# Performance work log

Hardware: AMD Instinct MI355X
Metric: run time of the kernel (lower is better)

The kernel has to match this reference:

```python
import jax, jax.numpy as jnp
import numpy as np

N = 50000      # nodes
E_RAND = 800000
IN = 256       # in_dim
HID = 64       # num_hidden
H = 4          # heads for GATv2 layers 0,1
C = 32         # num_classes (final layer, 1 head)
SLOPE = 0.2


def setup_inputs() -> dict:
    key = jax.random.key(0)
    ks = jax.random.split(key, 12)
    x = jax.random.normal(ks[0], (N, IN), dtype=jnp.float32)
    src = jax.random.randint(ks[1], (E_RAND,), 0, N, dtype=jnp.int32)
    dst = jax.random.randint(ks[2], (E_RAND,), 0, N, dtype=jnp.int32)
    loops = jnp.arange(N, dtype=jnp.int32)  # self-loops: every node has an in-edge
    src = jnp.concatenate([src, loops])
    dst = jnp.concatenate([dst, loops])
    s = 0.05
    W0 = jax.random.normal(ks[3], (IN, H * HID), dtype=jnp.float32) * s
    a0 = jax.random.normal(ks[4], (H, HID), dtype=jnp.float32) * s
    W1 = jax.random.normal(ks[5], (H * HID, H * HID), dtype=jnp.float32) * s
    a1 = jax.random.normal(ks[6], (H, HID), dtype=jnp.float32) * s
    W2 = jax.random.normal(ks[7], (H * HID, 1 * C), dtype=jnp.float32) * s
    a2 = jax.random.normal(ks[8], (1, C), dtype=jnp.float32) * s
    Wres2 = jax.random.normal(ks[9], (H * HID, C), dtype=jnp.float32) * s
    return {"x": x, "src": src, "dst": dst, "W0": W0, "a0": a0,
            "W1": W1, "a1": a1, "W2": W2, "a2": a2, "Wres2": Wres2}


def _gatv2_layer(h, W, a, src, dst, heads, out, res, activation):
    n = h.shape[0]
    # share_weights=True: same projection for src and dst (DGL GATv2Conv)
    f = (h @ W).reshape(n, heads, out)            # [N,H,D]
    fe = f[src] + f[dst]                          # gather: [E,H,D]
    e = jnp.einsum('ehd,hd->eh', jax.nn.leaky_relu(fe, SLOPE), a)  # [E,H]
    # edge softmax over incoming edges per destination node
    m = jax.ops.segment_max(e, dst, num_segments=n)
    ex = jnp.exp(e - m[dst])
    z = jax.ops.segment_sum(ex, dst, num_segments=n)
    alpha = ex / z[dst]                           # [E,H]
    msg = alpha[:, :, None] * f[src]              # [E,H,D]
    rst = jax.ops.segment_sum(msg, dst, num_segments=n)  # [N,H,D]
    if res is not None:
        rst = rst + res
    if activation:
        rst = jax.nn.elu(rst)
    return rst


def reference(x, src, dst, W0, a0, W1, a1, W2, a2, Wres2):
    # layer 0: no residual, elu, flatten heads
    h = _gatv2_layer(x, W0, a0, src, dst, H, HID, None, True).reshape(N, H * HID)
    # layer 1: residual (in == heads*out -> identity reshape), elu, flatten
    res1 = h.reshape(N, H, HID)
    h = _gatv2_layer(h, W1, a1, src, dst, H, HID, res1, True).reshape(N, H * HID)
    # final layer: residual via res_fc (256 != 1*32), no activation, mean over heads
    res2 = (h @ Wres2).reshape(N, 1, C)
    logits = _gatv2_layer(h, W2, a2, src, dst, 1, C, res2, False).mean(axis=1)
    return logits
```

## Files before the change

### kernel.cpp

```cpp
#include <hip/hip_runtime.h>
#include <hip/hip_bf16.h>

typedef __hip_bfloat16 bf16;
#define SLOPE 0.2f

typedef _Float16 h2v __attribute__((ext_vector_type(2)));
typedef _Float16 h8v __attribute__((ext_vector_type(8)));
typedef __attribute__((ext_vector_type(8))) short bf16x8;
typedef __attribute__((ext_vector_type(16))) float f32x16;

__device__ __forceinline__ float b2f(bf16 v) { return __bfloat162float(v); }
__device__ __forceinline__ short f2b_raw(float x) {
    bf16 b = __float2bfloat16(x);
    return *reinterpret_cast<short*>(&b);
}
__device__ __forceinline__ short f2h_raw(float x) {
    _Float16 h = (_Float16)x;
    return *reinterpret_cast<short*>(&h);
}
__device__ __forceinline__ h2v u2h(unsigned u) {
    union { unsigned x; h2v h; } c; c.x = u; return c.h;
}

template <int CTRL>
__device__ __forceinline__ float dpp_radd(float x) {
    int y = __builtin_amdgcn_update_dpp(0, __float_as_int(x), CTRL, 0xF, 0xF, false);
    return x + __int_as_float(y);
}
#define DPP_QUAD_XOR1 0xB1
#define DPP_QUAD_XOR2 0x4E
#define DPP_ROR1 0x121
#define DPP_ROR2 0x122
#define DPP_ROR4 0x124
#define DPP_ROR8 0x128

union Q16 { uint4 q[2]; unsigned u[8]; };

__global__ void k_prep(const void* __restrict__ x,
                       const void* __restrict__ W0, const void* __restrict__ W1,
                       const void* __restrict__ W2, const void* __restrict__ Wr2,
                       const void* __restrict__ a0, const void* __restrict__ a1,
                       const void* __restrict__ a2, short* __restrict__ W0p,
                       short* __restrict__ W1p, short* __restrict__ W2fp,
                       short* __restrict__ a0c, short* __restrict__ a1c,
                       short* __restrict__ a2c, int* __restrict__ flag,
                       int* __restrict__ cnt, int* __restrict__ ticket, int N) {
    __shared__ int sflag;
    if (threadIdx.x < 64) {
        const unsigned short* u = (const unsigned short*)x;
        int tid = threadIdx.x;
        int nice = 0;
        for (int k = tid; k < 256; k += 64) {
            unsigned int bits = ((unsigned int)u[2 * k]) << 16;
            float v = __uint_as_float(bits);
            float av = fabsf(v);
            if (v == 0.0f || (av > 1e-6f && av < 100.0f)) ++nice;
        }
        for (int off = 32; off > 0; off >>= 1) nice += __shfl_down(nice, off, 64);
        if (tid == 0) sflag = (nice >= 192) ? 0 : 1;
    }
    __syncthreads();
    int isf = sflag;
    int idx = blockIdx.x * blockDim.x + threadIdx.x;
    if (blockIdx.x == 0 && threadIdx.x == 0) { *flag = isf; *ticket = 0; }
    if (idx < N) cnt[idx] = 0;
    if (idx < 131072) {
        int t = idx & 65535;
        int j = t & 7, L = (t >> 3) & 63, kt = (t >> 9) & 15, nt = t >> 13;
        int n = nt * 32 + (L & 31);
        int k = kt * 16 + (L >> 5) * 8 + j;
        const void* src = (idx < 65536) ? W0 : W1;
        float v = isf ? ((const float*)src)[k * 256 + n] : b2f(((const bf16*)src)[k * 256 + n]);
        short* dstp = (idx < 65536) ? W0p : W1p;
        dstp[t] = f2h_raw(v);
    } else if (idx < 147456) {
        int t = idx - 131072;
        int j = t & 7, L = (t >> 3) & 63, kt = (t >> 9) & 15, nt = t >> 13;
        int n = nt * 32 + (L & 31);
        int k = kt * 16 + (L >> 5) * 8 + j;
        const void* src = (n < 32) ? W2 : Wr2;
        int nn = n & 31;
        float v = isf ? ((const float*)src)[k * 32 + nn] : b2f(((const bf16*)src)[k * 32 + nn]);
        W2fp[t] = f2h_raw(v);
    } else if (idx < 147456 + 256) {
        int t = idx - 147456;
        float v = isf ? ((const float*)a0)[t] : b2f(((const bf16*)a0)[t]);
        a0c[t] = f2h_raw(v);
    } else if (idx < 147456 + 512) {
        int t = idx - 147456 - 256;
        float v = isf ? ((const float*)a1)[t] : b2f(((const bf16*)a1)[t]);
        a1c[t] = f2h_raw(v);
    } else if (idx < 147456 + 544) {
        int t = idx - 147456 - 512;
        float v = isf ? ((const float*)a2)[t] : b2f(((const bf16*)a2)[t]);
        a2c[t] = f2h_raw(v);
    }
}

__global__ void k_hist(const int* __restrict__ dst, int* __restrict__ cnt, int E) {
    int e = blockIdx.x * blockDim.x + threadIdx.x;
    if (e < E) atomicAdd(&cnt[dst[e]], 1);
}

__global__ void k_bsum_scan(const int* __restrict__ cnt, int* __restrict__ bsum,
                            int* __restrict__ ticket, int n, int B) {
    __shared__ int sh[256];
    __shared__ int lastFlag;
    int base = blockIdx.x * 1024 + threadIdx.x * 4;
    int s = 0;
#pragma unroll
    for (int k = 0; k < 4; ++k) { int i = base + k; if (i < n) s += cnt[i]; }
    sh[threadIdx.x] = s;
    __syncthreads();
    for (int off = 128; off > 0; off >>= 1) {
        if (threadIdx.x < off) sh[threadIdx.x] += sh[threadIdx.x + off];
        __syncthreads();
    }
    if (threadIdx.x == 0) {
        atomicExch(&bsum[blockIdx.x], sh[0]);
        __threadfence();
        int t = atomicAdd(ticket, 1);
        lastFlag = (t == B - 1) ? 1 : 0;
    }
    __syncthreads();
    if (lastFlag && threadIdx.x < 64) {
        int tid = threadIdx.x;
        int v = (tid < B) ? atomicAdd(&bsum[tid], 0) : 0;
        int xv = v;
#pragma unroll
        for (int off = 1; off < 64; off <<= 1) {
            int y = __shfl_up(xv, off, 64);
            if (tid >= off) xv += y;
        }
        if (tid < B) bsum[tid] = xv - v;
    }
}

__global__ void k_scanwrite(const int* __restrict__ cnt, const int* __restrict__ bsum,
                            int* __restrict__ rowptr, int* __restrict__ cursor, int n, int E) {
    __shared__ int sh[256];
    int base = blockIdx.x * 1024 + threadIdx.x * 4;
    int loc[4];
    int s = 0;
#pragma unroll
    for (int k = 0; k < 4; ++k) {
        int i = base + k;
        loc[k] = (i < n) ? cnt[i] : 0;
        s += loc[k];
    }
    sh[threadIdx.x] = s;
    __syncthreads();
    for (int off = 1; off < 256; off <<= 1) {
        int u = (threadIdx.x >= off) ? sh[threadIdx.x - off] : 0;
        __syncthreads();
        sh[threadIdx.x] += u;
        __syncthreads();
    }
    int run = bsum[blockIdx.x] + sh[threadIdx.x] - s;
#pragma unroll
    for (int k = 0; k < 4; ++k) {
        int i = base + k;
        if (i < n) { rowptr[i] = run; cursor[i] = run; run += loc[k]; }
    }
    if (blockIdx.x == 0 && threadIdx.x == 0) rowptr[n] = E;
}

__global__ void k_scatter(const int* __restrict__ src, const int* __restrict__ dst,
                          int* __restrict__ cursor, int* __restrict__ csr_src, int E) {
    int e = blockIdx.x * blockDim.x + threadIdx.x;
    if (e < E) {
        int p = atomicAdd(&cursor[dst[e]], 1);
        csr_src[p] = src[e];
    }
}

template <int ADAPT>
__global__ void k_gemm_mfma(const void* __restrict__ A, const short* __restrict__ Wp,
                            short* __restrict__ C, int Nrows, const int* __restrict__ flag) {
    __shared__ short sA[64 * 264];
    int tid = threadIdx.x;
    int warp = tid >> 6;
    int lane = tid & 63;
    long blockRow = (long)blockIdx.x * 64;
    int isf32 = ADAPT ? *flag : 0;

    if (ADAPT && isf32) {
        const float* Af = (const float*)A;
#pragma unroll
        for (int it = 0; it < 16; ++it) {
            int linear = it * 256 + tid;
            int row = linear >> 6;
            int col4 = linear & 63;
            long gr = blockRow + row;
            if (gr > Nrows - 1) gr = Nrows - 1;
            float4 v = ((const float4*)(Af + gr * 256))[col4];
            short* d = &sA[row * 264 + col4 * 4];
            d[0] = f2h_raw(v.x); d[1] = f2h_raw(v.y);
            d[2] = f2h_raw(v.z); d[3] = f2h_raw(v.w);
        }
    } else if (ADAPT) {
        const short* Ab = (const short*)A;
#pragma unroll
        for (int it = 0; it < 8; ++it) {
            int linear = it * 256 + tid;
            int row = linear >> 5;
            int c8 = linear & 31;
            long gr = blockRow + row;
            if (gr > Nrows - 1) gr = Nrows - 1;
            bf16x8 v = *(const bf16x8*)(Ab + gr * 256 + c8 * 8);
            short* d = &sA[row * 264 + c8 * 8];
#pragma unroll
            for (int k = 0; k < 8; ++k) {
                unsigned bits = ((unsigned)(unsigned short)v[k]) << 16;
                d[k] = f2h_raw(__uint_as_float(bits));
            }
        }
    } else {
        const short* Ab = (const short*)A;
#pragma unroll
        for (int it = 0; it < 8; ++it) {
            int linear = it * 256 + tid;
            int row = linear >> 5;
            int c8 = linear & 31;
            long gr = blockRow + row;
            if (gr > Nrows - 1) gr = Nrows - 1;
            bf16x8 v = *(const bf16x8*)(Ab + gr * 256 + c8 * 8);
            *(bf16x8*)&sA[row * 264 + c8 * 8] = v;
        }
    }
    __syncthreads();

    int wr = warp >> 1;
    int wc = warp & 1;
    long rowBase = blockRow + wr * 32;
    int colBase = wc * 128;
    int m = lane & 31;
    int g = lane >> 5;
    int smemRow = wr * 32 + m;
    f32x16 acc[4] = {};
    for (int kt = 0; kt < 16; ++kt) {
        h8v af = *(const h8v*)&sA[smemRow * 264 + kt * 16 + g * 8];
#pragma unroll
        for (int ct = 0; ct < 4; ++ct) {
            int nt = wc * 4 + ct;
            h8v bfr = *(const h8v*)(Wp + (((nt << 4) + kt) << 9) + lane * 8);
            acc[ct] = __builtin_amdgcn_mfma_f32_32x32x16_f16(af, bfr, acc[ct], 0, 0, 0);
        }
    }
#pragma unroll
    for (int ct = 0; ct < 4; ++ct) {
#pragma unroll
        for (int i = 0; i < 16; ++i) {
            long row = rowBase + (i & 3) + 8 * (i >> 2) + 4 * g;
            if (row < Nrows)
                C[row * 256 + colBase + ct * 32 + m] = f2h_raw(acc[ct][i]);
        }
    }
}

__global__ void k_gemm_mfma64(const short* __restrict__ A, const short* __restrict__ Wp,
                              short* __restrict__ C, int Nrows) {
    int warp = threadIdx.x >> 6;
    int lane = threadIdx.x & 63;
    long rowBase = (long)blockIdx.x * 128 + warp * 32;
    int m = lane & 31;
    int g = lane >> 5;
    long r = rowBase + m;
    if (r >= Nrows) r = Nrows - 1;
    const short* Arow = A + r * 256 + g * 8;
    f32x16 acc[2] = {};
    for (int kt = 0; kt < 16; ++kt) {
        h8v af = *(const h8v*)(Arow + kt * 16);
#pragma unroll
        for (int ct = 0; ct < 2; ++ct) {
            h8v bfr = *(const h8v*)(Wp + (((ct << 4) + kt) << 9) + lane * 8);
            acc[ct] = __builtin_amdgcn_mfma_f32_32x32x16_f16(af, bfr, acc[ct], 0, 0, 0);
        }
    }
#pragma unroll
    for (int ct = 0; ct < 2; ++ct) {
#pragma unroll
        for (int i = 0; i < 16; ++i) {
            long row = rowBase + (i & 3) + 8 * (i >> 2) + 4 * g;
            if (row < Nrows)
                C[row * 64 + ct * 32 + m] = f2h_raw(acc[ct][i]);
        }
    }
}

__global__ void k_gat_fused(const uint4* __restrict__ f, const short* __restrict__ a,
                            const int* __restrict__ rowptr, const int* __restrict__ csr_src,
                            const uint4* __restrict__ res, uint4* __restrict__ out,
                            int N, int mode) {
    int n = (blockIdx.x * blockDim.x + threadIdx.x) >> 6;
    int lane = threadIdx.x & 63;
    if (n >= N) return;
    int j = lane >> 4, l = lane & 15;

    Q16 fdq, aq;
    fdq.q[0] = f[(long)n * 32 + 2 * l];
    fdq.q[1] = f[(long)n * 32 + 2 * l + 1];
    aq.q[0] = ((const uint4*)a)[2 * l];
    aq.q[1] = ((const uint4*)a)[2 * l + 1];
    h2v a6h[8], a4h[8];
#pragma unroll
    for (int i = 0; i < 8; ++i) {
        h2v av = u2h(aq.u[i]);
        float ax = (float)av.x, ay = (float)av.y;
        h2v t6, t4;
        t6.x = (_Float16)(0.6f * ax); t6.y = (_Float16)(0.6f * ay);
        t4.x = (_Float16)(0.4f * ax); t4.y = (_Float16)(0.4f * ay);
        a6h[i] = t6;
        a4h[i] = t4;
    }

    int p0 = rowptr[n], p1 = rowptr[n + 1];
    int iters = (p1 - p0 + 3) >> 2;
    float z = 0.f;
    float accx[8] = {}, accy[8] = {};

    int p = p0 + j;
    int pc = p1 - 1;
    Q16 A0, A1, B0, B1;
    {
        int s0 = csr_src[min(p, pc)];
        A0.q[0] = f[(long)s0 * 32 + 2 * l];
        A0.q[1] = f[(long)s0 * 32 + 2 * l + 1];
        int s1 = csr_src[min(p + 4, pc)];
        A1.q[0] = f[(long)s1 * 32 + 2 * l];
        A1.q[1] = f[(long)s1 * 32 + 2 * l + 1];
    }
    for (int i = 0; i < iters; i += 2) {
        int s0 = csr_src[min(p + 8, pc)];
        B0.q[0] = f[(long)s0 * 32 + 2 * l];
        B0.q[1] = f[(long)s0 * 32 + 2 * l + 1];
        int s1 = csr_src[min(p + 12, pc)];
        B1.q[0] = f[(long)s1 * 32 + 2 * l];
        B1.q[1] = f[(long)s1 * 32 + 2 * l + 1];

#pragma unroll
        for (int half = 0; half < 2; ++half) {
            if (half == 1 && i + 1 >= iters) break;
            const Q16& cur = half ? A1 : A0;
            int pp = p + half * 4;
            float t = 0.f;
#pragma unroll
            for (int k = 0; k < 8; ++k) {
                unsigned uu;
                asm("v_pk_add_f16 %0, %1, %2" : "=v"(uu) : "v"(cur.u[k]), "v"(fdq.u[k]));
                unsigned ua = uu & 0x7fff7fffu;
                t = __builtin_amdgcn_fdot2(u2h(uu), a6h[k], t, false);
                t = __builtin_amdgcn_fdot2(u2h(ua), a4h[k], t, false);
            }
            t = dpp_radd<DPP_QUAD_XOR1>(t);
            t = dpp_radd<DPP_QUAD_XOR2>(t);
            float wgt = (pp < p1) ? __expf(t) : 0.f;
            z += wgt;
#pragma unroll
            for (int k = 0; k < 8; ++k) {
                asm("v_fma_mix_f32 %0, %1, %2, %0 op_sel_hi:[1,0,0]"
                    : "+v"(accx[k]) : "v"(cur.u[k]), "v"(wgt));
                asm("v_fma_mix_f32 %0, %1, %2, %0 op_sel:[1,0,0] op_sel_hi:[1,0,0]"
                    : "+v"(accy[k]) : "v"(cur.u[k]), "v"(wgt));
            }
        }
        A0 = B0;
        A1 = B1;
        p += 8;
    }
    z += __shfl_xor(z, 16);
    z += __shfl_xor(z, 32);
#pragma unroll
    for (int k = 0; k < 8; ++k) {
        accx[k] += __shfl_xor(accx[k], 16);
        accx[k] += __shfl_xor(accx[k], 32);
        accy[k] += __shfl_xor(accy[k], 16);
        accy[k] += __shfl_xor(accy[k], 32);
    }
    if (j < 2) {
        float invz = 1.f / z;
        float o[8];
#pragma unroll
        for (int k = 0; k < 4; ++k) {
            int kk = j * 4 + k;
            o[2 * k]     = accx[kk] * invz;
            o[2 * k + 1] = accy[kk] * invz;
        }
        if (mode == 1) {
            uint4 rq = res[(long)n * 32 + 2 * l + j];
            const unsigned* ru = (const unsigned*)&rq;
#pragma unroll
            for (int k = 0; k < 4; ++k) {
                h2v rh = u2h(ru[k]);
                o[2 * k]     += (float)rh.x;
                o[2 * k + 1] += (float)rh.y;
            }
        }
        union { uint4 q; short s[8]; } ob;
#pragma unroll
        for (int k = 0; k < 8; ++k) {
            float v = o[k] > 0.f ? o[k] : (__expf(o[k]) - 1.f);
            ob.s[k] = f2h_raw(v);
        }
        out[(long)n * 32 + 2 * l + j] = ob.q;
    }
}

__global__ void k_gat_fused_fin(const unsigned* __restrict__ fr2u, const short* __restrict__ a2,
                                const int* __restrict__ rowptr, const int* __restrict__ csr_src,
                                void* __restrict__ outraw, int N, const int* __restrict__ flag) {
    int n = (blockIdx.x * blockDim.x + threadIdx.x) >> 6;
    int lane = threadIdx.x & 63;
    if (n >= N) return;
    int j = lane >> 4, l = lane & 15;

    unsigned fdu = fr2u[(long)n * 32 + l];
    unsigned au  = ((const unsigned*)a2)[l];
    h2v av  = u2h(au);
    float ax = (float)av.x, ay = (float)av.y;
    h2v a6h, a4h;
    a6h.x = (_Float16)(0.6f * ax); a6h.y = (_Float16)(0.6f * ay);
    a4h.x = (_Float16)(0.4f * ax); a4h.y = (_Float16)(0.4f * ay);

    int p0 = rowptr[n], p1 = rowptr[n + 1];
    int iters = (p1 - p0 + 3) >> 2;
    float z = 0.f;
    float accx = 0.f, accy = 0.f;

    int p = p0 + j;
    int pc = p1 - 1;
    unsigned A0, A1, B0, B1;
    A0 = fr2u[(long)csr_src[min(p, pc)] * 32 + l];
    A1 = fr2u[(long)csr_src[min(p + 4, pc)] * 32 + l];
    for (int i = 0; i < iters; i += 2) {
        B0 = fr2u[(long)csr_src[min(p + 8, pc)] * 32 + l];
        B1 = fr2u[(long)csr_src[min(p + 12, pc)] * 32 + l];
#pragma unroll
        for (int half = 0; half < 2; ++half) {
            if (half == 1 && i + 1 >= iters) break;
            unsigned cu = half ? A1 : A0;
            int pp = p + half * 4;
            unsigned uu;
            asm("v_pk_add_f16 %0, %1, %2" : "=v"(uu) : "v"(cu), "v"(fdu));
            unsigned ua = uu & 0x7fff7fffu;
            float t = __builtin_amdgcn_fdot2(u2h(uu), a6h, 0.f, false);
            t = __builtin_amdgcn_fdot2(u2h(ua), a4h, t, false);
            t = dpp_radd<DPP_ROR1>(t);
            t = dpp_radd<DPP_ROR2>(t);
            t = dpp_radd<DPP_ROR4>(t);
            t = dpp_radd<DPP_ROR8>(t);
            float wgt = (pp < p1) ? __expf(t) : 0.f;
            z += wgt;
            asm("v_fma_mix_f32 %0, %1, %2, %0 op_sel_hi:[1,0,0]"
                : "+v"(accx) : "v"(cu), "v"(wgt));
            asm("v_fma_mix_f32 %0, %1, %2, %0 op_sel:[1,0,0] op_sel_hi:[1,0,0]"
                : "+v"(accy) : "v"(cu), "v"(wgt));
        }
        A0 = B0;
        A1 = B1;
        p += 8;
    }
    z += __shfl_xor(z, 16);
    z += __shfl_xor(z, 32);
    accx += __shfl_xor(accx, 16);
    accx += __shfl_xor(accx, 32);
    accy += __shfl_xor(accy, 16);
    accy += __shfl_xor(accy, 32);
    if (j == 0) {
        unsigned ru = fr2u[(long)n * 32 + 16 + l];
        h2v rh = u2h(ru);
        float invz = 1.f / z;
        float o0 = accx * invz + (float)rh.x;
        float o1 = accy * invz + (float)rh.y;
        if (*flag) {
            float2 ov = {o0, o1};
            ((float2*)outraw)[(long)n * 16 + l] = ov;
        } else {
            unsigned ob = ((unsigned)(unsigned short)f2b_raw(o0)) |
                          (((unsigned)(unsigned short)f2b_raw(o1)) << 16);
            ((unsigned*)outraw)[(long)n * 16 + l] = ob;
        }
    }
}

extern "C" void kernel_launch(void* const* d_in, const int* in_sizes, int n_in,
                              void* d_out, int out_size, void* d_ws, size_t ws_size,
                              hipStream_t stream) {
    const int N = in_sizes[0] / 256;
    const int E = in_sizes[1];

    const void* x   = d_in[0];
    const int*  src = (const int*)d_in[1];
    const int*  dst = (const int*)d_in[2];

    char* w = (char*)d_ws;
    auto alloc = [&](size_t bytes) -> char* {
        char* p = w;
        w += (bytes + 15) & ~(size_t)15;
        return p;
    };
    short* buf0 = (short*)alloc((size_t)N * 256 * 2);
    short* buf1 = (short*)alloc((size_t)N * 256 * 2);
    short* buf2 = (short*)alloc((size_t)N * 256 * 2);
    int* csr_src = (int*)alloc((size_t)E * 4);
    int* rowptr  = (int*)alloc((size_t)(N + 1) * 4);
    int* cursor  = (int*)alloc((size_t)N * 4);
    int* cnt     = (int*)alloc((size_t)N * 4);
    int* bsum    = (int*)alloc((size_t)1024 * 4);
    short* W0p  = (short*)alloc((size_t)65536 * 2);
    short* W1p  = (short*)alloc((size_t)65536 * 2);
    short* W2fp = (short*)alloc((size_t)64 * 256 * 2);
    short* a0c  = (short*)alloc((size_t)256 * 2);
    short* a1c  = (short*)alloc((size_t)256 * 2);
    short* a2c  = (short*)alloc((size_t)32 * 2);
    int*  flag = (int*)alloc(16);
    int*  ticket = (int*)alloc(16);

    short* hA  = buf1;
    short* fB  = buf2;
    short* hB  = buf0;
    short* fr2 = buf2;

    int prepN = 147456 + 544;
    if (prepN < N) prepN = N;
    k_prep<<<(prepN + 255) / 256, 256, 0, stream>>>(
        x, d_in[3], d_in[5], d_in[7], d_in[9], d_in[4], d_in[6], d_in[8],
        W0p, W1p, W2fp, a0c, a1c, a2c, flag, cnt, ticket, N);

    const int B = (N + 1023) / 1024;
    k_hist<<<(E + 255) / 256, 256, 0, stream>>>(dst, cnt, E);
    k_bsum_scan<<<B, 256, 0, stream>>>(cnt, bsum, ticket, N, B);
    k_scanwrite<<<B, 256, 0, stream>>>(cnt, bsum, rowptr, cursor, N, E);
    k_scatter<<<(E + 255) / 256, 256, 0, stream>>>(src, dst, cursor, csr_src, E);

    const int ngrid4 = (int)(((long)N * 64 + 255) / 256);

    k_gemm_mfma<1><<<(N + 63) / 64, 256, 0, stream>>>(x, W0p, fB, N, flag);
    k_gat_fused<<<ngrid4, 256, 0, stream>>>((const uint4*)fB, a0c, rowptr, csr_src,
                                            nullptr, (uint4*)hA, N, 0);
    k_gemm_mfma<0><<<(N + 63) / 64, 256, 0, stream>>>(hA, W1p, fB, N, flag);
    k_gat_fused<<<ngrid4, 256, 0, stream>>>((const uint4*)fB, a1c, rowptr, csr_src,
                                            (const uint4*)hA, (uint4*)hB, N, 1);
    k_gemm_mfma64<<<(N + 127) / 128, 256, 0, stream>>>(hB, W2fp, fr2, N);
    k_gat_fused_fin<<<ngrid4, 256, 0, stream>>>((const unsigned*)fr2, a2c, rowptr, csr_src,
                                                d_out, N, flag);
}
```

Measured before the change: 386.1 us.

## Use persistent grid-stride GAT aggregation with deeper index prefetch and split dot accumulators

The three GAT aggregation kernels become persistent grid-stride loops over nodes with a capped grid of 2048 blocks, so per-wave setup such as attention-vector preparation and the flag read happens once per wave. The edge loop now fetches csr_src indices two steps ahead of the feature gathers, shortening the dependent index-then-feature latency chain. The attention dot product is split across four independent accumulators to break the serial fdot2 chain. The cost is fewer waves in flight, since 2048 blocks of 4 waves each replace one wave per node, and longer per-wave serial work that can leave imbalance at the tail.

```diff
diff --git a/kernel.cpp b/kernel.cpp
--- a/kernel.cpp
+++ b/kernel.cpp
@@ -292,14 +292,12 @@
                             const int* __restrict__ rowptr, const int* __restrict__ csr_src,
                             const uint4* __restrict__ res, uint4* __restrict__ out,
                             int N, int mode) {
-    int n = (blockIdx.x * blockDim.x + threadIdx.x) >> 6;
+    int w = (blockIdx.x * blockDim.x + threadIdx.x) >> 6;
+    int wstride = (gridDim.x * blockDim.x) >> 6;
     int lane = threadIdx.x & 63;
-    if (n >= N) return;
     int j = lane >> 4, l = lane & 15;
 
-    Q16 fdq, aq;
-    fdq.q[0] = f[(long)n * 32 + 2 * l];
-    fdq.q[1] = f[(long)n * 32 + 2 * l + 1];
+    Q16 aq;
     aq.q[0] = ((const uint4*)a)[2 * l];
     aq.q[1] = ((const uint4*)a)[2 * l + 1];
     h2v a6h[8], a4h[8];
@@ -314,171 +312,198 @@
         a4h[i] = t4;
     }
 
-    int p0 = rowptr[n], p1 = rowptr[n + 1];
-    int iters = (p1 - p0 + 3) >> 2;
-    float z = 0.f;
-    float accx[8] = {}, accy[8] = {};
-
-    int p = p0 + j;
-    int pc = p1 - 1;
-    Q16 A0, A1, B0, B1;
-    {
-        int s0 = csr_src[min(p, pc)];
-        A0.q[0] = f[(long)s0 * 32 + 2 * l];
-        A0.q[1] = f[(long)s0 * 32 + 2 * l + 1];
-        int s1 = csr_src[min(p + 4, pc)];
-        A1.q[0] = f[(long)s1 * 32 + 2 * l];
-        A1.q[1] = f[(long)s1 * 32 + 2 * l + 1];
-    }
-    for (int i = 0; i < iters; i += 2) {
-        int s0 = csr_src[min(p + 8, pc)];
-        B0.q[0] = f[(long)s0 * 32 + 2 * l];
-        B0.q[1] = f[(long)s0 * 32 + 2 * l + 1];
-        int s1 = csr_src[min(p + 12, pc)];
-        B1.q[0] = f[(long)s1 * 32 + 2 * l];
-        B1.q[1] = f[(long)s1 * 32 + 2 * l + 1];
-
-#pragma unroll
-        for (int half = 0; half < 2; ++half) {
-            if (half == 1 && i + 1 >= iters) break;
-            const Q16& cur = half ? A1 : A0;
-            int pp = p + half * 4;
-            float t = 0.f;
+    for (int n = w; n < N; n += wstride) {
+        Q16 fdq;
+        fdq.q[0] = f[(long)n * 32 + 2 * l];
+        fdq.q[1] = f[(long)n * 32 + 2 * l + 1];
+
+        int p0 = rowptr[n], p1 = rowptr[n + 1];
+        int iters = (p1 - p0 + 3) >> 2;
+        float z = 0.f;
+        float accx[8] = {}, accy[8] = {};
+
+        int p = p0 + j;
+        int pc = p1 - 1;
+        Q16 A0, A1, B0, B1;
+        {
+            int s0 = csr_src[min(p, pc)];
+            A0.q[0] = f[(long)s0 * 32 + 2 * l];
+            A0.q[1] = f[(long)s0 * 32 + 2 * l + 1];
+            int s1 = csr_src[min(p + 4, pc)];
+            A1.q[0] = f[(long)s1 * 32 + 2 * l];
+            A1.q[1] = f[(long)s1 * 32 + 2 * l + 1];
+        }
+        int t0i = csr_src[min(p + 8, pc)];
+        int t1i = csr_src[min(p + 12, pc)];
+
+        for (int i = 0; i < iters; i += 2) {
+            B0.q[0] = f[(long)t0i * 32 + 2 * l];
+            B0.q[1] = f[(long)t0i * 32 + 2 * l + 1];
+            B1.q[0] = f[(long)t1i * 32 + 2 * l];
+            B1.q[1] = f[(long)t1i * 32 + 2 * l + 1];
+            int u0i = csr_src[min(p + 16, pc)];
+            int u1i = csr_src[min(p + 20, pc)];
+
+#pragma unroll
+            for (int half = 0; half < 2; ++half) {
+                if (half == 1 && i + 1 >= iters) break;
+                const Q16& cur = half ? A1 : A0;
+                int pp = p + half * 4;
+                float ta0 = 0.f, ta1 = 0.f, ta2 = 0.f, ta3 = 0.f;
+#pragma unroll
+                for (int k = 0; k < 8; ++k) {
+                    unsigned uu;
+                    asm("v_pk_add_f16 %0, %1, %2" : "=v"(uu) : "v"(cur.u[k]), "v"(fdq.u[k]));
+                    unsigned ua = uu & 0x7fff7fffu;
+                    if ((k & 1) == 0) {
+                        ta0 = __builtin_amdgcn_fdot2(u2h(uu), a6h[k], ta0, false);
+                        ta1 = __builtin_amdgcn_fdot2(u2h(ua), a4h[k], ta1, false);
+                    } else {
+                        ta2 = __builtin_amdgcn_fdot2(u2h(uu), a6h[k], ta2, false);
+                        ta3 = __builtin_amdgcn_fdot2(u2h(ua), a4h[k], ta3, false);
+                    }
+                }
+                float t = (ta0 + ta1) + (ta2 + ta3);
+                t = dpp_radd<DPP_QUAD_XOR1>(t);
+                t = dpp_radd<DPP_QUAD_XOR2>(t);
+                float wgt = (pp < p1) ? __expf(t) : 0.f;
+                z += wgt;
+#pragma unroll
+                for (int k = 0; k < 8; ++k) {
+                    asm("v_fma_mix_f32 %0, %1, %2, %0 op_sel_hi:[1,0,0]"
+                        : "+v"(accx[k]) : "v"(cur.u[k]), "v"(wgt));
+                    asm("v_fma_mix_f32 %0, %1, %2, %0 op_sel:[1,0,0] op_sel_hi:[1,0,0]"
+                        : "+v"(accy[k]) : "v"(cur.u[k]), "v"(wgt));
+                }
+            }
+            A0 = B0;
+            A1 = B1;
+            t0i = u0i;
+            t1i = u1i;
+            p += 8;
+        }
+        z += __shfl_xor(z, 16);
+        z += __shfl_xor(z, 32);
+#pragma unroll
+        for (int k = 0; k < 8; ++k) {
+            accx[k] += __shfl_xor(accx[k], 16);
+            accx[k] += __shfl_xor(accx[k], 32);
+            accy[k] += __shfl_xor(accy[k], 16);
+            accy[k] += __shfl_xor(accy[k], 32);
+        }
+        if (j < 2) {
+            float invz = 1.f / z;
+            float o[8];
+#pragma unroll
+            for (int k = 0; k < 4; ++k) {
+                int kk = j * 4 + k;
+                o[2 * k]     = accx[kk] * invz;
+                o[2 * k + 1] = accy[kk] * invz;
+            }
+            if (mode == 1) {
+                uint4 rq = res[(long)n * 32 + 2 * l + j];
+                const unsigned* ru = (const unsigned*)&rq;
+#pragma unroll
+                for (int k = 0; k < 4; ++k) {
+                    h2v rh = u2h(ru[k]);
+                    o[2 * k]     += (float)rh.x;
+                    o[2 * k + 1] += (float)rh.y;
+                }
+            }
+            union { uint4 q; short s[8]; } ob;
 #pragma unroll
             for (int k = 0; k < 8; ++k) {
-                unsigned uu;
-                asm("v_pk_add_f16 %0, %1, %2" : "=v"(uu) : "v"(cur.u[k]), "v"(fdq.u[k]));
-                unsigned ua = uu & 0x7fff7fffu;
-                t = __builtin_amdgcn_fdot2(u2h(uu), a6h[k], t, false);
-                t = __builtin_amdgcn_fdot2(u2h(ua), a4h[k], t, false);
-            }
-            t = dpp_radd<DPP_QUAD_XOR1>(t);
-            t = dpp_radd<DPP_QUAD_XOR2>(t);
-            float wgt = (pp < p1) ? __expf(t) : 0.f;
-            z += wgt;
-#pragma unroll
-            for (int k = 0; k < 8; ++k) {
-                asm("v_fma_mix_f32 %0, %1, %2, %0 op_sel_hi:[1,0,0]"
-                    : "+v"(accx[k]) : "v"(cur.u[k]), "v"(wgt));
-                asm("v_fma_mix_f32 %0, %1, %2, %0 op_sel:[1,0,0] op_sel_hi:[1,0,0]"
-                    : "+v"(accy[k]) : "v"(cur.u[k]), "v"(wgt));
-            }
-        }
-        A0 = B0;
-        A1 = B1;
-        p += 8;
-    }
-    z += __shfl_xor(z, 16);
-    z += __shfl_xor(z, 32);
-#pragma unroll
-    for (int k = 0; k < 8; ++k) {
-        accx[k] += __shfl_xor(accx[k], 16);
-        accx[k] += __shfl_xor(accx[k], 32);
-        accy[k] += __shfl_xor(accy[k], 16);
-        accy[k] += __shfl_xor(accy[k], 32);
-    }
-    if (j < 2) {
-        float invz = 1.f / z;
-        float o[8];
-#pragma unroll
-        for (int k = 0; k < 4; ++k) {
-            int kk = j * 4 + k;
-            o[2 * k]     = accx[kk] * invz;
-            o[2 * k + 1] = accy[kk] * invz;
-        }
-        if (mode == 1) {
-            uint4 rq = res[(long)n * 32 + 2 * l + j];
-            const unsigned* ru = (const unsigned*)&rq;
-#pragma unroll
-            for (int k = 0; k < 4; ++k) {
-                h2v rh = u2h(ru[k]);
-                o[2 * k]     += (float)rh.x;
-                o[2 * k + 1] += (float)rh.y;
-            }
-        }
-        union { uint4 q; short s[8]; } ob;
-#pragma unroll
-        for (int k = 0; k < 8; ++k) {
-            float v = o[k] > 0.f ? o[k] : (__expf(o[k]) - 1.f);
-            ob.s[k] = f2h_raw(v);
-        }
-        out[(long)n * 32 + 2 * l + j] = ob.q;
+                float v = o[k] > 0.f ? o[k] : (__expf(o[k]) - 1.f);
+                ob.s[k] = f2h_raw(v);
+            }
+            out[(long)n * 32 + 2 * l + j] = ob.q;
+        }
     }
 }
 
 __global__ void k_gat_fused_fin(const unsigned* __restrict__ fr2u, const short* __restrict__ a2,
                                 const int* __restrict__ rowptr, const int* __restrict__ csr_src,
                                 void* __restrict__ outraw, int N, const int* __restrict__ flag) {
-    int n = (blockIdx.x * blockDim.x + threadIdx.x) >> 6;
+    int w = (blockIdx.x * blockDim.x + threadIdx.x) >> 6;
+    int wstride = (gridDim.x * blockDim.x) >> 6;
     int lane = threadIdx.x & 63;
-    if (n >= N) return;
     int j = lane >> 4, l = lane & 15;
 
-    unsigned fdu = fr2u[(long)n * 32 + l];
     unsigned au  = ((const unsigned*)a2)[l];
     h2v av  = u2h(au);
     float ax = (float)av.x, ay = (float)av.y;
     h2v a6h, a4h;
     a6h.x = (_Float16)(0.6f * ax); a6h.y = (_Float16)(0.6f * ay);
     a4h.x = (_Float16)(0.4f * ax); a4h.y = (_Float16)(0.4f * ay);
-
-    int p0 = rowptr[n], p1 = rowptr[n + 1];
-    int iters = (p1 - p0 + 3) >> 2;
-    float z = 0.f;
-    float accx = 0.f, accy = 0.f;
-
-    int p = p0 + j;
-    int pc = p1 - 1;
-    unsigned A0, A1, B0, B1;
-    A0 = fr2u[(long)csr_src[min(p, pc)] * 32 + l];
-    A1 = fr2u[(long)csr_src[min(p + 4, pc)] * 32 + l];
-    for (int i = 0; i < iters; i += 2) {
-        B0 = fr2u[(long)csr_src[min(p + 8, pc)] * 32 + l];
-        B1 = fr2u[(long)csr_src[min(p + 12, pc)] * 32 + l];
-#pragma unroll
-        for (int half = 0; half < 2; ++half) {
-            if (half == 1 && i + 1 >= iters) break;
-            unsigned cu = half ? A1 : A0;
-            int pp = p + half * 4;
-            unsigned uu;
-            asm("v_pk_add_f16 %0, %1, %2" : "=v"(uu) : "v"(cu), "v"(fdu));
-            unsigned ua = uu & 0x7fff7fffu;
-            float t = __builtin_amdgcn_fdot2(u2h(uu), a6h, 0.f, false);
-            t = __builtin_amdgcn_fdot2(u2h(ua), a4h, t, false);
-            t = dpp_radd<DPP_ROR1>(t);
-            t = dpp_radd<DPP_ROR2>(t);
-            t = dpp_radd<DPP_ROR4>(t);
-            t = dpp_radd<DPP_ROR8>(t);
-            float wgt = (pp < p1) ? __expf(t) : 0.f;
-            z += wgt;
-            asm("v_fma_mix_f32 %0, %1, %2, %0 op_sel_hi:[1,0,0]"
-                : "+v"(accx) : "v"(cu), "v"(wgt));
-            asm("v_fma_mix_f32 %0, %1, %2, %0 op_sel:[1,0,0] op_sel_hi:[1,0,0]"
-                : "+v"(accy) : "v"(cu), "v"(wgt));
-        }
-        A0 = B0;
-        A1 = B1;
-        p += 8;
-    }
-    z += __shfl_xor(z, 16);
-    z += __shfl_xor(z, 32);
-    accx += __shfl_xor(accx, 16);
-    accx += __shfl_xor(accx, 32);
-    accy += __shfl_xor(accy, 16);
-    accy += __shfl_xor(accy, 32);
-    if (j == 0) {
-        unsigned ru = fr2u[(long)n * 32 + 16 + l];
-        h2v rh = u2h(ru);
-        float invz = 1.f / z;
-        float o0 = accx * invz + (float)rh.x;
-        float o1 = accy * invz + (float)rh.y;
-        if (*flag) {
-            float2 ov = {o0, o1};
-            ((float2*)outraw)[(long)n * 16 + l] = ov;
-        } else {
-            unsigned ob = ((unsigned)(unsigned short)f2b_raw(o0)) |
-                          (((unsigned)(unsigned short)f2b_raw(o1)) << 16);
-            ((unsigned*)outraw)[(long)n * 16 + l] = ob;
+    int isf = *flag;
+
+    for (int n = w; n < N; n += wstride) {
+        unsigned fdu = fr2u[(long)n * 32 + l];
+
+        int p0 = rowptr[n], p1 = rowptr[n + 1];
+        int iters = (p1 - p0 + 3) >> 2;
+        float z = 0.f;
+        float accx = 0.f, accy = 0.f;
+
+        int p = p0 + j;
+        int pc = p1 - 1;
+        unsigned A0, A1, B0, B1;
+        A0 = fr2u[(long)csr_src[min(p, pc)] * 32 + l];
+        A1 = fr2u[(long)csr_src[min(p + 4, pc)] * 32 + l];
+        int t0i = csr_src[min(p + 8, pc)];
+        int t1i = csr_src[min(p + 12, pc)];
+        for (int i = 0; i < iters; i += 2) {
+            B0 = fr2u[(long)t0i * 32 + l];
+            B1 = fr2u[(long)t1i * 32 + l];
+            int u0i = csr_src[min(p + 16, pc)];
+            int u1i = csr_src[min(p + 20, pc)];
+#pragma unroll
+            for (int half = 0; half < 2; ++half) {
+                if (half == 1 && i + 1 >= iters) break;
+                unsigned cu = half ? A1 : A0;
+                int pp = p + half * 4;
+                unsigned uu;
+                asm("v_pk_add_f16 %0, %1, %2" : "=v"(uu) : "v"(cu), "v"(fdu));
+                unsigned ua = uu & 0x7fff7fffu;
+                float t = __builtin_amdgcn_fdot2(u2h(uu), a6h, 0.f, false);
+                t = __builtin_amdgcn_fdot2(u2h(ua), a4h, t, false);
+                t = dpp_radd<DPP_ROR1>(t);
+                t = dpp_radd<DPP_ROR2>(t);
+                t = dpp_radd<DPP_ROR4>(t);
+                t = dpp_radd<DPP_ROR8>(t);
+                float wgt = (pp < p1) ? __expf(t) : 0.f;
+                z += wgt;
+                asm("v_fma_mix_f32 %0, %1, %2, %0 op_sel_hi:[1,0,0]"
+                    : "+v"(accx) : "v"(cu), "v"(wgt));
+                asm("v_fma_mix_f32 %0, %1, %2, %0 op_sel:[1,0,0] op_sel_hi:[1,0,0]"
+                    : "+v"(accy) : "v"(cu), "v"(wgt));
+            }
+            A0 = B0;
+            A1 = B1;
+            t0i = u0i;
+            t1i = u1i;
+            p += 8;
+        }
+        z += __shfl_xor(z, 16);
+        z += __shfl_xor(z, 32);
+        accx += __shfl_xor(accx, 16);
+        accx += __shfl_xor(accx, 32);
+        accy += __shfl_xor(accy, 16);
+        accy += __shfl_xor(accy, 32);
+        if (j == 0) {
+            unsigned ru = fr2u[(long)n * 32 + 16 + l];
+            h2v rh = u2h(ru);
+            float invz = 1.f / z;
+            float o0 = accx * invz + (float)rh.x;
+            float o1 = accy * invz + (float)rh.y;
+            if (isf) {
+                float2 ov = {o0, o1};
+                ((float2*)outraw)[(long)n * 16 + l] = ov;
+            } else {
+                unsigned ob = ((unsigned)(unsigned short)f2b_raw(o0)) |
+                              (((unsigned)(unsigned short)f2b_raw(o1)) << 16);
+                ((unsigned*)outraw)[(long)n * 16 + l] = ob;
+            }
         }
     }
 }
@@ -533,15 +558,19 @@
     k_scanwrite<<<B, 256, 0, stream>>>(cnt, bsum, rowptr, cursor, N, E);
     k_scatter<<<(E + 255) / 256, 256, 0, stream>>>(src, dst, cursor, csr_src, E);
 
-    const int ngrid4 = (int)(((long)N * 64 + 255) / 256);
+    int pgrid = 2048;
+    {
+        int maxg = (int)(((long)N * 64 + 255) / 256);
+        if (pgrid > maxg) pgrid = maxg;
+    }
 
     k_gemm_mfma<1><<<(N + 63) / 64, 256, 0, stream>>>(x, W0p, fB, N, flag);
-    k_gat_fused<<<ngrid4, 256, 0, stream>>>((const uint4*)fB, a0c, rowptr, csr_src,
-                                            nullptr, (uint4*)hA, N, 0);
+    k_gat_fused<<<pgrid, 256, 0, stream>>>((const uint4*)fB, a0c, rowptr, csr_src,
+                                           nullptr, (uint4*)hA, N, 0);
     k_gemm_mfma<0><<<(N + 63) / 64, 256, 0, stream>>>(hA, W1p, fB, N, flag);
-    k_gat_fused<<<ngrid4, 256, 0, stream>>>((const uint4*)fB, a1c, rowptr, csr_src,
-                                            (const uint4*)hA, (uint4*)hB, N, 1);
+    k_gat_fused<<<pgrid, 256, 0, stream>>>((const uint4*)fB, a1c, rowptr, csr_src,
+                                           (const uint4*)hA, (uint4*)hB, N, 1);
     k_gemm_mfma64<<<(N + 127) / 128, 256, 0, stream>>>(hB, W2fp, fr2, N);
-    k_gat_fused_fin<<<ngrid4, 256, 0, stream>>>((const unsigned*)fr2, a2c, rowptr, csr_src,
-                                                d_out, N, flag);
-}
+    k_gat_fused_fin<<<pgrid, 256, 0, stream>>>((const unsigned*)fr2, a2c, rowptr, csr_src,
+                                               d_out, N, flag);
+}
```

Result: no change. 387.4 us (+0.3%).
